# Kernel tuning notes

Measured on AMD Instinct MI355X. Metric: run time of the kernel, lower is better.

Reference implementation:

```python
import jax, jax.numpy as jnp
import numpy as np

ALPHA = 0.05
MAX_ITER = 200
TOL = 0.01
N = 64
M = 1
BATCH = 262144


def setup_inputs() -> dict:
    key = jax.random.key(0)
    pred_cost = jax.random.normal(key, (BATCH, N), dtype=jnp.float32)
    # constraint data (fixed buffers, match init_kwargs)
    A = np.ones((M, N), dtype=np.float32)
    b = np.full((M,), 32.0, dtype=np.float32)
    lb = np.zeros((N,), dtype=np.float32)
    ub = np.ones((N,), dtype=np.float32)
    # SVD-based pseudoinverse factors for equality projection
    U, s, VT = np.linalg.svd(A, full_matrices=False)
    s_inv = np.where(s >= 1e-6, 1.0 / s, 0.0).astype(np.float32)
    return {
        "pred_cost": pred_cost,
        "A": jnp.asarray(A),
        "b": jnp.asarray(b),
        "lb": jnp.asarray(lb),
        "ub": jnp.asarray(ub),
        "V": jnp.asarray(VT.T.astype(np.float32)),   # (n, m)
        "UT": jnp.asarray(U.T.astype(np.float32)),   # (m, m)
        "s_inv": jnp.asarray(s_inv),                 # (m,)
    }


def _project_box(z, lb, ub):
    return jnp.clip(z, lb, ub)


def _project_equality(w, A, b, V, UT, s_inv):
    # w: (B, n). residual r = A w^T - b, correction = V diag(s_inv) U^T r
    r = w @ A.T - b                      # (B, m)
    corr = ((r @ UT.T) * s_inv) @ V.T    # (B, n)
    return w - corr


def _dys_step(z, cost, A, b, lb, ub, V, UT, s_inv):
    x = _project_box(z, lb, ub)
    grad = cost + ALPHA * x              # grad of regularized objective
    y = _project_equality(2.0 * x - z - ALPHA * grad, A, b, V, UT, s_inv)
    return z - x + y


def _run_to_convergence(cost, A, b, lb, ub, V, UT, s_inv):
    lb_safe = jnp.where(jnp.isfinite(lb), lb, 0.0)
    ub_safe = jnp.where(jnp.isfinite(ub), ub, 1.0)
    z0 = jax.random.uniform(jax.random.key(1), cost.shape, dtype=cost.dtype)
    z0 = z0 * (ub_safe - lb_safe) + lb_safe

    def cond(state):
        i, z, diff = state
        return jnp.logical_and(i < MAX_ITER, diff > TOL)

    def body(state):
        i, z, _ = state
        z_new = _dys_step(z, cost, A, b, lb, ub, V, UT, s_inv)
        diff = jnp.max(jnp.linalg.norm(z_new - z, axis=1))
        return (i + 1, z_new, diff)

    _, z, _ = jax.lax.while_loop(cond, body, (jnp.int32(0), z0, jnp.float32(1e30)))
    return z


def reference(pred_cost, A, b, lb, ub, V, UT, s_inv):
    cost = pred_cost  # minimize=True
    # no-grad fixed-point iterations
    z = jax.lax.stop_gradient(
        _run_to_convergence(jax.lax.stop_gradient(cost), A, b, lb, ub, V, UT, s_inv)
    )
    # training branch: one differentiable DYS step (JFB), then box projection
    z = _dys_step(z, cost, A, b, lb, ub, V, UT, s_inv)
    sol = _project_box(z, lb, ub)
    return sol
```

## Files before the change

### kernel.cpp

```cpp
#include <hip/hip_runtime.h>
#include <cstdint>


#ifndef JAX_PARTITIONABLE
#define JAX_PARTITIONABLE 1
#endif

#define BATCHN 262144
#define MAXIT  200
#define RPW    32
#define NWAVES (BATCHN / RPW)
#define PROBE_ROWS 8192
#define PROBE_WAVES (PROBE_ROWS / RPW)

#define K1 0.9975f
#define K2 1.9975f

__device__ __forceinline__ void tf2x32(uint32_t x0, uint32_t x1,
                                       uint32_t& o0, uint32_t& o1) {
  const uint32_t k0 = 0u, k1 = 1u;
  const uint32_t k2 = 0x1BD11BDAu ^ k0 ^ k1;
  x0 += k0; x1 += k1;
#define TFR(r) { x0 += x1; x1 = (x1 << (r)) | (x1 >> (32 - (r))); x1 ^= x0; }
  TFR(13) TFR(15) TFR(26) TFR(6)   x0 += k1; x1 += k2 + 1u;
  TFR(17) TFR(29) TFR(16) TFR(24)  x0 += k2; x1 += k0 + 2u;
  TFR(13) TFR(15) TFR(26) TFR(6)   x0 += k0; x1 += k1 + 3u;
  TFR(17) TFR(29) TFR(16) TFR(24)  x0 += k1; x1 += k2 + 4u;
  TFR(13) TFR(15) TFR(26) TFR(6)   x0 += k2; x1 += k0 + 5u;
#undef TFR
  o0 = x0; o1 = x1;
}

__device__ __forceinline__ float z0_at(uint32_t f) {
  uint32_t b;
#if JAX_PARTITIONABLE
  uint32_t o0, o1;
  tf2x32(0u, f, o0, o1);
  b = o0 ^ o1;
#else
  const uint32_t H = 8388608u;
  uint32_t lo = (f < H) ? f : (f - H);
  uint32_t o0, o1;
  tf2x32(lo, lo + H, o0, o1);
  b = (f < H) ? o0 : o1;
#endif
  return __uint_as_float((b >> 9) | 0x3f800000u) - 1.0f;
}

__device__ __forceinline__ void fast_iter(float U[32], const float c[32],
                                          float& CC, float& R) {
  const float Ch = CC + 20.0f;
  float g[8];
#pragma unroll
  for (int q = 0; q < 8; ++q) {
    float m0 = __builtin_amdgcn_fmed3f(U[4 * q + 0], CC, Ch);
    float m1 = __builtin_amdgcn_fmed3f(U[4 * q + 1], CC, Ch);
    float m2 = __builtin_amdgcn_fmed3f(U[4 * q + 2], CC, Ch);
    float m3 = __builtin_amdgcn_fmed3f(U[4 * q + 3], CC, Ch);
    U[4 * q + 0] = __builtin_fmaf(K1, m0, -c[4 * q + 0]);
    U[4 * q + 1] = __builtin_fmaf(K1, m1, -c[4 * q + 1]);
    U[4 * q + 2] = __builtin_fmaf(K1, m2, -c[4 * q + 2]);
    U[4 * q + 3] = __builtin_fmaf(K1, m3, -c[4 * q + 3]);
    g[q] = (m0 + m1) + (m2 + m3);
  }
  float s = ((g[0] + g[1]) + (g[2] + g[3])) + ((g[4] + g[5]) + (g[6] + g[7]));
  s += __shfl_xor(s, 1);
  float Sx = 0.05f * __builtin_fmaf(-64.0f, CC, s);
  float t  = __builtin_fmaf(K2, Sx, -R);
  float corr20 = __builtin_fmaf(t, 0.3125f, -10.0f);
  R = (R - Sx) + 32.0f;
  CC = __builtin_fmaf(K1, CC, corr20);
}

__device__ __forceinline__ float chk_iter(float U[32], const float c[32],
                                          float& CC, float& R) {
  const float Ch = CC + 20.0f;
  float g[8];
  float q1 = 0.0f, q2 = 0.0f;
#pragma unroll
  for (int q = 0; q < 8; ++q) {
    float m0 = __builtin_amdgcn_fmed3f(U[4 * q + 0], CC, Ch);
    float m1 = __builtin_amdgcn_fmed3f(U[4 * q + 1], CC, Ch);
    float m2 = __builtin_amdgcn_fmed3f(U[4 * q + 2], CC, Ch);
    float m3 = __builtin_amdgcn_fmed3f(U[4 * q + 3], CC, Ch);
    g[q] = (m0 + m1) + (m2 + m3);
#pragma unroll
    for (int e = 0; e < 4; ++e) {
      int j = 4 * q + e;
      float m = (e == 0) ? m0 : (e == 1) ? m1 : (e == 2) ? m2 : m3;
      float un = __builtin_fmaf(K1, m, -c[j]);
      float d = un - U[j];
      q1 += d;
      q2 = __builtin_fmaf(d, d, q2);
      U[j] = un;
    }
  }
  float s = ((g[0] + g[1]) + (g[2] + g[3])) + ((g[4] + g[5]) + (g[6] + g[7]));
  s += __shfl_xor(s, 1);
  float Sx = 0.05f * __builtin_fmaf(-64.0f, CC, s);
  float t  = __builtin_fmaf(K2, Sx, -R);
  float corr20 = __builtin_fmaf(t, 0.3125f, -10.0f);
  R = (R - Sx) + 32.0f;
  float CCn = __builtin_fmaf(K1, CC, corr20);
  float dCC = CCn - CC;
  CC = CCn;
  q1 += __shfl_xor(q1, 1);
  q2 += __shfl_xor(q2, 1);
  float a = __builtin_fmaf(64.0f, dCC, -2.0f * q1);
  return __builtin_fmaf(dCC, a, q2);
}

__device__ __forceinline__ void load_c(const float* __restrict__ cost,
                                       int base, float c[32]) {
#pragma unroll
  for (int k = 0; k < 8; ++k) {
    const float4 cq = *(const float4*)(cost + base + 4 * k);
    c[4 * k + 0] = cq.x; c[4 * k + 1] = cq.y;
    c[4 * k + 2] = cq.z; c[4 * k + 3] = cq.w;
  }
}

__device__ __forceinline__ void init_state(const float* __restrict__ cost,
                                           int base, float c[32], float U[32],
                                           float& CC, float& R) {
  load_c(cost, base, c);
  float r = 0.0f;
#pragma unroll
  for (int j = 0; j < 32; ++j) {
    float z0 = z0_at((uint32_t)(base + j));
    U[j] = 20.0f * z0;
    r = __builtin_fmaf(0.05f, c[j], r + z0);
  }
  r += __shfl_xor(r, 1);
  R = r;
  CC = 0.0f;
}

__global__ __launch_bounds__(256, 4) void dys_probe(
    const float* __restrict__ cost, int* __restrict__ Tsample) {
  const int lane = threadIdx.x & 63;
  const int gw = blockIdx.x * 4 + (threadIdx.x >> 6);
  const int base = (gw * RPW + (lane >> 1)) * 64 + (lane & 1) * 32;

  float c[32], U[32], CC, R;
  init_state(cost, base, c, U, CC, R);

  int ib = MAXIT;
  for (int i = 1; i <= MAXIT; ++i) {
    float ds = chk_iter(U, c, CC, R);
    if (__all(ds <= 0.04f)) { ib = i; break; }
  }
  if (lane == 0) atomicMax(Tsample, ib);
}

__global__ __launch_bounds__(256, 4) void dys_pass1(
    const float* __restrict__ cost, const int* __restrict__ Tsample,
    int* __restrict__ Tglob, int* __restrict__ TrArr,
    float* __restrict__ zst) {
  const int lane = threadIdx.x & 63;
  const int gw = blockIdx.x * 4 + (threadIdx.x >> 6);
  const int base = (gw * RPW + (lane >> 1)) * 64 + (lane & 1) * 32;

  float c[32], U[32], CC, R;
  init_state(cost, base, c, U, CC, R);

  const int Ts = *Tsample;
  const int P = (Ts > 2) ? (Ts - 2) : 0;

  for (int i = 0; i < P; ++i) fast_iter(U, c, CC, R);

  int ib = MAXIT;
  for (int i = P + 1; i <= MAXIT; ++i) {
    float ds = chk_iter(U, c, CC, R);
    if (__all(ds <= 0.04f)) { ib = i; break; }
  }

  const float CC05 = 0.05f * CC;
#pragma unroll
  for (int k = 0; k < 8; ++k) {
    float4 zq;
    zq.x = __builtin_fmaf(0.05f, U[4 * k + 0], -CC05);
    zq.y = __builtin_fmaf(0.05f, U[4 * k + 1], -CC05);
    zq.z = __builtin_fmaf(0.05f, U[4 * k + 2], -CC05);
    zq.w = __builtin_fmaf(0.05f, U[4 * k + 3], -CC05);
    *(float4*)(zst + base + 4 * k) = zq;
  }
  if (lane == 0) {
    TrArr[gw] = ib;
    atomicMax(Tglob, ib);
  }
}

__global__ __launch_bounds__(256, 4) void dys_pass2(
    const float* __restrict__ cost, const int* __restrict__ Tglob,
    const int* __restrict__ TrArr, const float* __restrict__ zst,
    float* __restrict__ out) {
  const int lane = threadIdx.x & 63;
  const int gw = blockIdx.x * 4 + (threadIdx.x >> 6);
  const int base = (gw * RPW + (lane >> 1)) * 64 + (lane & 1) * 32;

  float c[32], U[32];
  load_c(cost, base, c);
  float r = 0.0f;
#pragma unroll
  for (int k = 0; k < 8; ++k) {
    const float4 zq = *(const float4*)(zst + base + 4 * k);
    U[4 * k + 0] = 20.0f * zq.x; U[4 * k + 1] = 20.0f * zq.y;
    U[4 * k + 2] = 20.0f * zq.z; U[4 * k + 3] = 20.0f * zq.w;
    r += (zq.x + zq.y) + (zq.z + zq.w);
  }
#pragma unroll
  for (int j = 0; j < 32; ++j) r = __builtin_fmaf(0.05f, c[j], r);
  float CC = 0.0f;
  float R = r + __shfl_xor(r, 1);

  const int T = *Tglob;
  const int ib = TrArr[gw];

  for (int i = ib; i <= T; ++i) fast_iter(U, c, CC, R);

  const float CC05 = 0.05f * CC;
#pragma unroll
  for (int k = 0; k < 8; ++k) {
    float4 o;
    o.x = __builtin_amdgcn_fmed3f(
        __builtin_fmaf(0.05f, U[4 * k + 0], -CC05), 0.0f, 1.0f);
    o.y = __builtin_amdgcn_fmed3f(
        __builtin_fmaf(0.05f, U[4 * k + 1], -CC05), 0.0f, 1.0f);
    o.z = __builtin_amdgcn_fmed3f(
        __builtin_fmaf(0.05f, U[4 * k + 2], -CC05), 0.0f, 1.0f);
    o.w = __builtin_amdgcn_fmed3f(
        __builtin_fmaf(0.05f, U[4 * k + 3], -CC05), 0.0f, 1.0f);
    *(float4*)(out + base + 4 * k) = o;
  }
}

extern "C" void kernel_launch(void* const* d_in, const int* in_sizes, int n_in,
                              void* d_out, int out_size, void* d_ws,
                              size_t ws_size, hipStream_t stream) {
  const float* cost = (const float*)d_in[0];
  float* out = (float*)d_out;

  int* Tglob   = (int*)d_ws;
  int* Tsample = (int*)d_ws + 1;
  const size_t TR_OFF = 1024;
  const size_t Z_OFF  = TR_OFF + (size_t)NWAVES * sizeof(int);
  int*   TrArr = (int*)((char*)d_ws + TR_OFF);
  float* zst   = (float*)((char*)d_ws + Z_OFF);

  hipMemsetAsync(d_ws, 0, 8, stream);

  dim3 block(256);
  dys_probe<<<dim3(PROBE_WAVES / 4), block, 0, stream>>>(cost, Tsample);
  dys_pass1<<<dim3(NWAVES / 4), block, 0, stream>>>(cost, Tsample, Tglob,
                                                    TrArr, zst);
  dys_pass2<<<dim3(NWAVES / 4), block, 0, stream>>>(cost, Tglob, TrArr, zst,
                                                    out);
}
```

Baseline: 448.5 us.

## Split each row across four lanes and reduce with DPP instead of shuffles

Each 64-element row is now handled by four lanes holding 16 elements each instead of two lanes with 32, so a wave covers 16 rows. Cross-lane sums use DPP row moves (quad swaps) in place of ds_swizzle/shfl. Inline asm pins keep the state in VGPRs. This halves per-thread registers and the serial per-iteration dependency chain and doubles the number of waves, at the cost of more reduction steps per iteration and more redundant scalar work (CC/R updates) per row.

```diff
diff --git a/kernel.cpp b/kernel.cpp
--- a/kernel.cpp
+++ b/kernel.cpp
@@ -8,7 +8,7 @@
 
 #define BATCHN 262144
 #define MAXIT  200
-#define RPW    32
+#define RPW    16
 #define NWAVES (BATCHN / RPW)
 #define PROBE_ROWS 8192
 #define PROBE_WAVES (PROBE_ROWS / RPW)
@@ -47,24 +47,30 @@
   return __uint_as_float((b >> 9) | 0x3f800000u) - 1.0f;
 }
 
-__device__ __forceinline__ void fast_iter(float U[32], const float c[32],
+template <int CTRL>
+__device__ __forceinline__ float dpp_add(float v) {
+  int s = __builtin_amdgcn_mov_dpp(__float_as_int(v), CTRL, 0xF, 0xF, true);
+  return v + __int_as_float(s);
+}
+
+__device__ __forceinline__ float reduce4(float v) {
+  v = dpp_add<0xB1>(v);
+  v = dpp_add<0x4E>(v);
+  return v;
+}
+
+__device__ __forceinline__ void fast_iter(float U[16], const float c[16],
                                           float& CC, float& R) {
   const float Ch = CC + 20.0f;
-  float g[8];
-#pragma unroll
-  for (int q = 0; q < 8; ++q) {
-    float m0 = __builtin_amdgcn_fmed3f(U[4 * q + 0], CC, Ch);
-    float m1 = __builtin_amdgcn_fmed3f(U[4 * q + 1], CC, Ch);
-    float m2 = __builtin_amdgcn_fmed3f(U[4 * q + 2], CC, Ch);
-    float m3 = __builtin_amdgcn_fmed3f(U[4 * q + 3], CC, Ch);
-    U[4 * q + 0] = __builtin_fmaf(K1, m0, -c[4 * q + 0]);
-    U[4 * q + 1] = __builtin_fmaf(K1, m1, -c[4 * q + 1]);
-    U[4 * q + 2] = __builtin_fmaf(K1, m2, -c[4 * q + 2]);
-    U[4 * q + 3] = __builtin_fmaf(K1, m3, -c[4 * q + 3]);
-    g[q] = (m0 + m1) + (m2 + m3);
-  }
-  float s = ((g[0] + g[1]) + (g[2] + g[3])) + ((g[4] + g[5]) + (g[6] + g[7]));
-  s += __shfl_xor(s, 1);
+  float sp[4] = {0.0f, 0.0f, 0.0f, 0.0f};
+#pragma unroll
+  for (int j = 0; j < 16; ++j) {
+    float m = __builtin_amdgcn_fmed3f(U[j], CC, Ch);
+    sp[j & 3] += m;
+    U[j] = __builtin_fmaf(K1, m, -c[j]);
+  }
+  float s = (sp[0] + sp[1]) + (sp[2] + sp[3]);
+  s = reduce4(s);
   float Sx = 0.05f * __builtin_fmaf(-64.0f, CC, s);
   float t  = __builtin_fmaf(K2, Sx, -R);
   float corr20 = __builtin_fmaf(t, 0.3125f, -10.0f);
@@ -72,31 +78,23 @@
   CC = __builtin_fmaf(K1, CC, corr20);
 }
 
-__device__ __forceinline__ float chk_iter(float U[32], const float c[32],
+__device__ __forceinline__ float chk_iter(float U[16], const float c[16],
                                           float& CC, float& R) {
   const float Ch = CC + 20.0f;
-  float g[8];
-  float q1 = 0.0f, q2 = 0.0f;
-#pragma unroll
-  for (int q = 0; q < 8; ++q) {
-    float m0 = __builtin_amdgcn_fmed3f(U[4 * q + 0], CC, Ch);
-    float m1 = __builtin_amdgcn_fmed3f(U[4 * q + 1], CC, Ch);
-    float m2 = __builtin_amdgcn_fmed3f(U[4 * q + 2], CC, Ch);
-    float m3 = __builtin_amdgcn_fmed3f(U[4 * q + 3], CC, Ch);
-    g[q] = (m0 + m1) + (m2 + m3);
-#pragma unroll
-    for (int e = 0; e < 4; ++e) {
-      int j = 4 * q + e;
-      float m = (e == 0) ? m0 : (e == 1) ? m1 : (e == 2) ? m2 : m3;
-      float un = __builtin_fmaf(K1, m, -c[j]);
-      float d = un - U[j];
-      q1 += d;
-      q2 = __builtin_fmaf(d, d, q2);
-      U[j] = un;
-    }
-  }
-  float s = ((g[0] + g[1]) + (g[2] + g[3])) + ((g[4] + g[5]) + (g[6] + g[7]));
-  s += __shfl_xor(s, 1);
+  float sp[4] = {0.0f, 0.0f, 0.0f, 0.0f};
+  float q1a = 0.0f, q1b = 0.0f, q2a = 0.0f, q2b = 0.0f;
+#pragma unroll
+  for (int j = 0; j < 16; ++j) {
+    float m = __builtin_amdgcn_fmed3f(U[j], CC, Ch);
+    sp[j & 3] += m;
+    float un = __builtin_fmaf(K1, m, -c[j]);
+    float d = un - U[j];
+    if (j & 1) { q1b += d; q2b = __builtin_fmaf(d, d, q2b); }
+    else       { q1a += d; q2a = __builtin_fmaf(d, d, q2a); }
+    U[j] = un;
+  }
+  float s = (sp[0] + sp[1]) + (sp[2] + sp[3]);
+  s = reduce4(s);
   float Sx = 0.05f * __builtin_fmaf(-64.0f, CC, s);
   float t  = __builtin_fmaf(K2, Sx, -R);
   float corr20 = __builtin_fmaf(t, 0.3125f, -10.0f);
@@ -104,35 +102,41 @@
   float CCn = __builtin_fmaf(K1, CC, corr20);
   float dCC = CCn - CC;
   CC = CCn;
-  q1 += __shfl_xor(q1, 1);
-  q2 += __shfl_xor(q2, 1);
+  float q1 = reduce4(q1a + q1b);
+  float q2 = reduce4(q2a + q2b);
   float a = __builtin_fmaf(64.0f, dCC, -2.0f * q1);
   return __builtin_fmaf(dCC, a, q2);
 }
 
 __device__ __forceinline__ void load_c(const float* __restrict__ cost,
-                                       int base, float c[32]) {
-#pragma unroll
-  for (int k = 0; k < 8; ++k) {
+                                       int base, float c[16]) {
+#pragma unroll
+  for (int k = 0; k < 4; ++k) {
     const float4 cq = *(const float4*)(cost + base + 4 * k);
     c[4 * k + 0] = cq.x; c[4 * k + 1] = cq.y;
     c[4 * k + 2] = cq.z; c[4 * k + 3] = cq.w;
   }
 }
 
+__device__ __forceinline__ void pin16(float v[16]) {
+#pragma unroll
+  for (int j = 0; j < 16; ++j) asm("" : "+v"(v[j]));
+}
+
 __device__ __forceinline__ void init_state(const float* __restrict__ cost,
-                                           int base, float c[32], float U[32],
+                                           int base, float c[16], float U[16],
                                            float& CC, float& R) {
   load_c(cost, base, c);
   float r = 0.0f;
 #pragma unroll
-  for (int j = 0; j < 32; ++j) {
+  for (int j = 0; j < 16; ++j) {
     float z0 = z0_at((uint32_t)(base + j));
     U[j] = 20.0f * z0;
     r = __builtin_fmaf(0.05f, c[j], r + z0);
   }
-  r += __shfl_xor(r, 1);
-  R = r;
+  pin16(c);
+  pin16(U);
+  R = reduce4(r);
   CC = 0.0f;
 }
 
@@ -140,9 +144,9 @@
     const float* __restrict__ cost, int* __restrict__ Tsample) {
   const int lane = threadIdx.x & 63;
   const int gw = blockIdx.x * 4 + (threadIdx.x >> 6);
-  const int base = (gw * RPW + (lane >> 1)) * 64 + (lane & 1) * 32;
-
-  float c[32], U[32], CC, R;
+  const int base = (gw * RPW + (lane >> 2)) * 64 + (lane & 3) * 16;
+
+  float c[16], U[16], CC, R;
   init_state(cost, base, c, U, CC, R);
 
   int ib = MAXIT;
@@ -159,9 +163,9 @@
     float* __restrict__ zst) {
   const int lane = threadIdx.x & 63;
   const int gw = blockIdx.x * 4 + (threadIdx.x >> 6);
-  const int base = (gw * RPW + (lane >> 1)) * 64 + (lane & 1) * 32;
-
-  float c[32], U[32], CC, R;
+  const int base = (gw * RPW + (lane >> 2)) * 64 + (lane & 3) * 16;
+
+  float c[16], U[16], CC, R;
   init_state(cost, base, c, U, CC, R);
 
   const int Ts = *Tsample;
@@ -177,7 +181,7 @@
 
   const float CC05 = 0.05f * CC;
 #pragma unroll
-  for (int k = 0; k < 8; ++k) {
+  for (int k = 0; k < 4; ++k) {
     float4 zq;
     zq.x = __builtin_fmaf(0.05f, U[4 * k + 0], -CC05);
     zq.y = __builtin_fmaf(0.05f, U[4 * k + 1], -CC05);
@@ -197,22 +201,24 @@
     float* __restrict__ out) {
   const int lane = threadIdx.x & 63;
   const int gw = blockIdx.x * 4 + (threadIdx.x >> 6);
-  const int base = (gw * RPW + (lane >> 1)) * 64 + (lane & 1) * 32;
-
-  float c[32], U[32];
+  const int base = (gw * RPW + (lane >> 2)) * 64 + (lane & 3) * 16;
+
+  float c[16], U[16];
   load_c(cost, base, c);
   float r = 0.0f;
 #pragma unroll
-  for (int k = 0; k < 8; ++k) {
+  for (int k = 0; k < 4; ++k) {
     const float4 zq = *(const float4*)(zst + base + 4 * k);
     U[4 * k + 0] = 20.0f * zq.x; U[4 * k + 1] = 20.0f * zq.y;
     U[4 * k + 2] = 20.0f * zq.z; U[4 * k + 3] = 20.0f * zq.w;
     r += (zq.x + zq.y) + (zq.z + zq.w);
   }
 #pragma unroll
-  for (int j = 0; j < 32; ++j) r = __builtin_fmaf(0.05f, c[j], r);
+  for (int j = 0; j < 16; ++j) r = __builtin_fmaf(0.05f, c[j], r);
+  pin16(c);
+  pin16(U);
   float CC = 0.0f;
-  float R = r + __shfl_xor(r, 1);
+  float R = reduce4(r);
 
   const int T = *Tglob;
   const int ib = TrArr[gw];
@@ -221,7 +227,7 @@
 
   const float CC05 = 0.05f * CC;
 #pragma unroll
-  for (int k = 0; k < 8; ++k) {
+  for (int k = 0; k < 4; ++k) {
     float4 o;
     o.x = __builtin_amdgcn_fmed3f(
         __builtin_fmaf(0.05f, U[4 * k + 0], -CC05), 0.0f, 1.0f);
```

Result: faster. 408.6 us (-8.9%).
